# Kernel optimization log

Hardware: AMD Instinct MI355X
Metric: run time of the kernel (lower is better)

## Reference

```python
import jax, jax.numpy as jnp
import numpy as np

D = 1024      # d_model
H = 16        # num_heads
DK = D // H   # head dim = 64
C = 64        # chunk_size
MRP = 2 * C   # max_rel_pos = 128
B, S = 2, 2048


def setup_inputs() -> dict:
    key = jax.random.key(0)
    ks = jax.random.split(key, 7)
    s = 0.02
    x = jax.random.normal(ks[0], (B, S, D), jnp.float32)
    Wq = jax.random.normal(ks[1], (D, D), jnp.float32) * s
    Wk = jax.random.normal(ks[2], (D, D), jnp.float32) * s
    Wv = jax.random.normal(ks[3], (D, D), jnp.float32) * s
    Wo = jax.random.normal(ks[4], (D, D), jnp.float32) * s
    bq = jnp.zeros((D,), jnp.float32)
    bk = jnp.zeros((D,), jnp.float32)
    bv = jnp.zeros((D,), jnp.float32)
    bo = jnp.zeros((D,), jnp.float32)
    # torch init is zeros; use small values so the bias path is exercised
    rel_bias = jax.random.normal(ks[5], (2 * MRP + 1, H), jnp.float32) * s
    return dict(x=x, Wq=Wq, bq=bq, Wk=Wk, bk=bk, Wv=Wv, bv=bv, Wo=Wo, bo=bo,
                rel_bias=rel_bias)


def reference(x, Wq, bq, Wk, bk, Wv, bv, Wo, bo, rel_bias):
    b, s, _ = x.shape

    def heads(w, bias):
        return (x @ w + bias).reshape(b, s, H, DK).transpose(0, 2, 1, 3)  # [B,H,S,dk]

    Q = heads(Wq, bq)
    K = heads(Wk, bk)
    V = heads(Wv, bv)

    scale = jnp.sqrt(jnp.asarray(DK, x.dtype))
    scores = jnp.einsum('bhqd,bhkd->bhqk', Q, K) / scale  # [B,H,S,S]

    pos = jnp.arange(s)
    # chunked path's rel index reduces to global (q - k), clamped
    rel = jnp.clip(pos[:, None] - pos[None, :], -MRP, MRP) + MRP  # [S,S]
    bias2 = rel_bias[rel].transpose(2, 0, 1)  # [H,S,S]
    scores = scores + bias2[None]

    # growing-window chunk mask: query chunk i sees key chunks 0..i
    qc = pos // C
    allowed = qc[None, :] <= qc[:, None]  # [S_q, S_k]
    scores = jnp.where(allowed[None, None], scores, -jnp.inf)

    attn = jax.nn.softmax(scores, axis=-1)
    out = jnp.einsum('bhqk,bhkd->bhqd', attn, V)
    out = out.transpose(0, 2, 1, 3).reshape(b, s, D)
    return out @ Wo + bo
```

## Files before the change

### kernel.cpp

```cpp
#include <hip/hip_runtime.h>
#include <stdint.h>

#define NH 16
#define DKH 64
#define SEQ 2048
#define NBATCH 2
#define NROW (NBATCH*SEQ)
#define DM 1024
#define LOG2E 1.44269504088896f

typedef __attribute__((ext_vector_type(8))) __bf16 bf16x8;
typedef __attribute__((ext_vector_type(4))) __bf16 bf16x4;
typedef __attribute__((ext_vector_type(4))) float f32x4;

#if __has_builtin(__builtin_amdgcn_exp2f)
#define EXP2(x) __builtin_amdgcn_exp2f(x)
#else
#define EXP2(x) exp2f(x)
#endif

__device__ __forceinline__ unsigned short f2bf(float f) {
  union { float f; uint32_t u; } v; v.f = f;
  uint32_t r = v.u + 0x7FFFu + ((v.u >> 16) & 1u);
  return (unsigned short)(r >> 16);
}
__device__ __forceinline__ f32x4 mfma16(bf16x8 a, bf16x8 b, f32x4 c) {
  return __builtin_amdgcn_mfma_f32_16x16x32_bf16(a, b, c, 0, 0, 0);
}
__device__ __forceinline__ void gload_lds16(const void* g, void* l) {
  __builtin_amdgcn_global_load_lds(
      (__attribute__((address_space(1))) uint32_t*)(uintptr_t)g,
      (__attribute__((address_space(3))) uint32_t*)(uintptr_t)l,
      16, 0, 0);
}
__device__ __forceinline__ void barrier_raw() {
  asm volatile("" ::: "memory");
  __builtin_amdgcn_s_barrier();
  asm volatile("" ::: "memory");
}

__global__ __launch_bounds__(256) void k_cvt_x(const float* __restrict__ x,
                                               unsigned short* __restrict__ xb) {
  int i = blockIdx.x * 256 + threadIdx.x;
  float4 v = ((const float4*)x)[i];
  ushort4 o;
  o.x = f2bf(v.x); o.y = f2bf(v.y); o.z = f2bf(v.z); o.w = f2bf(v.w);
  ((ushort4*)xb)[i] = o;
}

__global__ __launch_bounds__(256) void k_cvt_w(
    const float* __restrict__ Wq, const float* __restrict__ Wk,
    const float* __restrict__ Wv, const float* __restrict__ Wo,
    unsigned short* __restrict__ Wqt, unsigned short* __restrict__ Wkt,
    unsigned short* __restrict__ Wvt, unsigned short* __restrict__ Wot) {
  __shared__ float tile[32][33];
  int z = blockIdx.z;
  const float* W = (z == 0) ? Wq : (z == 1) ? Wk : (z == 2) ? Wv : Wo;
  int ti = blockIdx.x, tj = blockIdx.y;
  int c = threadIdx.x & 31, r0 = threadIdx.x >> 5;
#pragma unroll
  for (int rr = 0; rr < 4; ++rr) {
    int r = r0 + rr * 8;
    tile[r][c] = W[(ti * 32 + r) * DM + tj * 32 + c];
  }
  __syncthreads();
  unsigned short* Out = (z == 0) ? Wqt : (z == 1) ? Wkt : (z == 2) ? Wvt : Wot;
#pragma unroll
  for (int rr = 0; rr < 4; ++rr) {
    int a = r0 + rr * 8;
    float v = tile[c][a];
    Out[(tj * 32 + a) * DM + ti * 32 + c] = f2bf(v);
  }
}

__global__ __launch_bounds__(256) void k_gemm_qkv(
    const unsigned short* __restrict__ xb,
    const unsigned short* __restrict__ Wqt, const unsigned short* __restrict__ Wkt,
    const unsigned short* __restrict__ Wvt,
    const float* __restrict__ bq, const float* __restrict__ bk,
    const float* __restrict__ bv,
    unsigned short* __restrict__ Q, unsigned short* __restrict__ Ko,
    unsigned short* __restrict__ Vt) {
  __shared__ __align__(16) unsigned short Al[2][128 * 64];
  __shared__ __align__(16) unsigned short Bl[2][128 * 64];
  int z = blockIdx.z;
  const unsigned short* Wt = (z == 0) ? Wqt : (z == 1) ? Wkt : Wvt;
  const float* bias = (z == 0) ? bq : (z == 1) ? bk : bv;

  int m0 = blockIdx.x * 128, n0 = blockIdx.y * 128;
  int tid = threadIdx.x, lane = tid & 63, wave = tid >> 6;
  int wr = wave >> 1, wc = wave & 1;
  int l15 = lane & 15, lg = lane >> 4;
  int r3 = lane >> 3, s3 = lane & 7;
  int gsw = (s3 ^ r3) << 4;
  int swz = l15 & 7;

  f32x4 acc[4][4] = {};

  auto stage = [&](int kb, int b) {
#pragma unroll
    for (int c = 0; c < 4; ++c) {
      int rb = c * 32 + wave * 8;
      gload_lds16((const char*)xb + (size_t)(m0 + rb + r3) * 2048 + kb * 128 + gsw,
                  (char*)&Al[b][0] + rb * 128);
      gload_lds16((const char*)Wt + (size_t)(n0 + rb + r3) * 2048 + kb * 128 + gsw,
                  (char*)&Bl[b][0] + rb * 128);
    }
  };

  stage(0, 0);
  stage(1, 1);

  for (int kb = 0; kb < 16; ++kb) {
    if (kb < 15) asm volatile("s_waitcnt vmcnt(8)" ::: "memory");
    else         asm volatile("s_waitcnt vmcnt(0)" ::: "memory");
    barrier_raw();
    int b = kb & 1;
#pragma unroll
    for (int ks = 0; ks < 2; ++ks) {
      int slot = lg + 4 * ks;
      int sofs = ((slot ^ swz) << 4);
      bf16x8 a[4], bfr[4];
#pragma unroll
      for (int mt = 0; mt < 4; ++mt)
        a[mt] = *(const bf16x8*)((const char*)&Al[b][0] + (wr * 64 + mt * 16 + l15) * 128 + sofs);
#pragma unroll
      for (int nt = 0; nt < 4; ++nt)
        bfr[nt] = *(const bf16x8*)((const char*)&Bl[b][0] + (wc * 64 + nt * 16 + l15) * 128 + sofs);
#pragma unroll
      for (int mt = 0; mt < 4; ++mt)
#pragma unroll
        for (int nt = 0; nt < 4; ++nt)
          acc[mt][nt] = mfma16(a[mt], bfr[nt], acc[mt][nt]);
    }
    barrier_raw();
    if (kb < 14) stage(kb + 2, b);
  }

#pragma unroll
  for (int nt = 0; nt < 4; ++nt) {
    int n = n0 + wc * 64 + nt * 16 + l15;
    float bb = bias[n];
    int h = n >> 6, dk = n & 63;
#pragma unroll
    for (int mt = 0; mt < 4; ++mt) {
      int mbase = m0 + wr * 64 + mt * 16 + lg * 4;
      int bidx = mbase >> 11, s = mbase & 2047;
      if (z < 2) {
        unsigned short* Out = (z == 0) ? Q : Ko;
#pragma unroll
        for (int r = 0; r < 4; ++r)
          Out[(((size_t)(bidx * NH + h)) * SEQ + s + r) * DKH + dk] =
              f2bf(acc[mt][nt][r] + bb);
      } else {
        ushort4 pk;
        pk.x = f2bf(acc[mt][nt][0] + bb);
        pk.y = f2bf(acc[mt][nt][1] + bb);
        pk.z = f2bf(acc[mt][nt][2] + bb);
        pk.w = f2bf(acc[mt][nt][3] + bb);
        *(ushort4*)&Vt[((size_t)(bidx * NH + h) * DKH + dk) * SEQ + s] = pk;
      }
    }
  }
}

__global__ __launch_bounds__(256) void k_attn(
    const unsigned short* __restrict__ Qg, const unsigned short* __restrict__ Kg,
    const unsigned short* __restrict__ Vtg, const float* __restrict__ rel_bias,
    unsigned short* __restrict__ AOh) {
  __shared__ __align__(16) unsigned short Kl[2][64 * 64];
  __shared__ __align__(16) unsigned short Vl[2][64 * 64];
  __shared__ float biasl[257];

  int blk = blockIdx.x;
  int bh = blk & 31;
  int qc = 31 - (blk >> 5);
  int h = bh & 15, bidx = bh >> 4;
  int tid = threadIdx.x, lane = tid & 63, wave = tid >> 6;
  int l15 = lane & 15, lg = lane >> 4;
  int r3 = lane >> 3, s3 = lane & 7;
  int gsw = (s3 ^ r3) * 16;

  const float C1L = 0.125f * LOG2E;

  for (int i = tid; i < 257; i += 256)
    biasl[i] = rel_bias[i * NH + h] * LOG2E - 6.0f * LOG2E;

  int qrow = qc * 64 + wave * 16 + l15;
  const unsigned short* qptr = Qg + ((size_t)bh * SEQ + qrow) * DKH + lg * 8;
  bf16x8 qf0 = *(const bf16x8*)(qptr);
  bf16x8 qf1 = *(const bf16x8*)(qptr + 32);

  const char* kcb = (const char*)(Kg + (size_t)bh * SEQ * DKH);
  const char* vcb = (const char*)(Vtg + (size_t)bh * DKH * SEQ);

  auto stage = [&](int j, int b) {
    const char* kj = kcb + (size_t)j * (64 * DKH * 2);
    const char* vj = vcb + (size_t)j * 128;
#pragma unroll
    for (int c = 0; c < 2; ++c) {
      int rb = wave * 16 + c * 8;
      gload_lds16(kj + (size_t)(rb + r3) * 128 + gsw,
                  (char*)&Kl[b][0] + rb * 128);
      gload_lds16(vj + (size_t)(rb + r3) * (SEQ * 2) + gsw,
                  (char*)&Vl[b][0] + rb * 128);
    }
  };

  float lsum = 0.f;
  f32x4 acc[4] = {};

  stage(0, 0);
  __syncthreads();
  float cfar = biasl[256];
  int swz = (l15 & 7);

  int vo[4];
#pragma unroll
  for (int kt = 0; kt < 4; ++kt)
    vo[kt] = (((kt * 2 + (lg >> 1)) ^ swz) << 4) + ((lg & 1) << 3);

  for (int j = 0; j <= qc; ++j) {
    int cur = j & 1;
    if (j < qc) stage(j + 1, cur ^ 1);

    const char* Kc = (const char*)&Kl[cur][0];
    const char* Vc = (const char*)&Vl[cur][0];

    f32x4 sa[4] = {};
    __builtin_amdgcn_s_setprio(1);
#pragma unroll
    for (int ks = 0; ks < 2; ++ks) {
      bf16x8 qa = ks ? qf1 : qf0;
      int slot = lg + 4 * ks;
#pragma unroll
      for (int kt = 0; kt < 4; ++kt) {
        bf16x8 kfr = *(const bf16x8*)(Kc + (kt * 16 + l15) * 128 + ((slot ^ swz) * 16));
        sa[kt] = mfma16(kfr, qa, sa[kt]);
      }
    }
    __builtin_amdgcn_s_setprio(0);

    float p[4][4];
    if (j >= qc - 2) {
      int kb0 = j * 64 + lg * 4;
#pragma unroll
      for (int kt = 0; kt < 4; ++kt)
#pragma unroll
        for (int r = 0; r < 4; ++r) {
          int rel = qrow - (kb0 + kt * 16 + r);
          rel = min(max(rel, -128), 128) + 128;
          p[kt][r] = EXP2(fmaf(sa[kt][r], C1L, biasl[rel]));
        }
    } else {
#pragma unroll
      for (int kt = 0; kt < 4; ++kt)
#pragma unroll
        for (int r = 0; r < 4; ++r)
          p[kt][r] = EXP2(fmaf(sa[kt][r], C1L, cfar));
    }
#pragma unroll
    for (int kt = 0; kt < 4; ++kt)
      lsum += (p[kt][0] + p[kt][1]) + (p[kt][2] + p[kt][3]);

    bf16x8 pfr0, pfr1;
#pragma unroll
    for (int jj = 0; jj < 4; ++jj) {
      pfr0[jj]     = (__bf16)p[0][jj];
      pfr0[jj + 4] = (__bf16)p[1][jj];
      pfr1[jj]     = (__bf16)p[2][jj];
      pfr1[jj + 4] = (__bf16)p[3][jj];
    }

    __builtin_amdgcn_s_setprio(1);
#pragma unroll
    for (int dt = 0; dt < 4; ++dt) {
      const char* vrow = Vc + (dt * 16 + l15) * 128;
      uint2 t0 = *(const uint2*)(vrow + vo[0]);
      uint2 t1 = *(const uint2*)(vrow + vo[1]);
      uint2 t2 = *(const uint2*)(vrow + vo[2]);
      uint2 t3 = *(const uint2*)(vrow + vo[3]);
      uint4 w0, w1;
      w0.x = t0.x; w0.y = t0.y; w0.z = t1.x; w0.w = t1.y;
      w1.x = t2.x; w1.y = t2.y; w1.z = t3.x; w1.w = t3.y;
      acc[dt] = mfma16(pfr0, *(const bf16x8*)&w0, acc[dt]);
      acc[dt] = mfma16(pfr1, *(const bf16x8*)&w1, acc[dt]);
    }
    __builtin_amdgcn_s_setprio(0);

    __syncthreads();
  }

  lsum += __shfl_xor(lsum, 16);
  lsum += __shfl_xor(lsum, 32);

#pragma unroll
  for (int r = 0; r < 4; ++r) {
    float inv = 1.0f / __shfl(lsum, lg * 4 + r, 64);
    int s = qc * 64 + wave * 16 + lg * 4 + r;
    size_t row = (size_t)bidx * SEQ + s;
#pragma unroll
    for (int dt = 0; dt < 4; ++dt) {
      float v = acc[dt][r] * inv;
      int col = h * 64 + dt * 16 + l15;
      AOh[row * DM + col] = f2bf(v);
    }
  }
}

__global__ __launch_bounds__(256) void k_gemm_out(
    const unsigned short* __restrict__ Ab, const unsigned short* __restrict__ Bt,
    const float* __restrict__ bo, float* __restrict__ out) {
  __shared__ __align__(16) unsigned short Al[2][128 * 64];
  __shared__ __align__(16) unsigned short Bl[2][128 * 64];

  int m0 = blockIdx.x * 128, n0 = blockIdx.y * 128;
  int tid = threadIdx.x, lane = tid & 63, wave = tid >> 6;
  int wr = wave >> 1, wc = wave & 1;
  int l15 = lane & 15, lg = lane >> 4;
  int r3 = lane >> 3, s3 = lane & 7;
  int gsw = (s3 ^ r3) << 4;
  int swz = l15 & 7;

  f32x4 acc[4][4] = {};

  auto stage = [&](int kb, int b) {
#pragma unroll
    for (int c = 0; c < 4; ++c) {
      int rb = c * 32 + wave * 8;
      gload_lds16((const char*)Ab + (size_t)(m0 + rb + r3) * 2048 + kb * 128 + gsw,
                  (char*)&Al[b][0] + rb * 128);
      gload_lds16((const char*)Bt + (size_t)(n0 + rb + r3) * 2048 + kb * 128 + gsw,
                  (char*)&Bl[b][0] + rb * 128);
    }
  };

  stage(0, 0);
  stage(1, 1);

  for (int kb = 0; kb < 16; ++kb) {
    if (kb < 15) asm volatile("s_waitcnt vmcnt(8)" ::: "memory");
    else         asm volatile("s_waitcnt vmcnt(0)" ::: "memory");
    barrier_raw();
    int b = kb & 1;
#pragma unroll
    for (int ks = 0; ks < 2; ++ks) {
      int slot = lg + 4 * ks;
      int sofs = ((slot ^ swz) << 4);
      bf16x8 a[4], bfr[4];
#pragma unroll
      for (int mt = 0; mt < 4; ++mt)
        a[mt] = *(const bf16x8*)((const char*)&Al[b][0] + (wr * 64 + mt * 16 + l15) * 128 + sofs);
#pragma unroll
      for (int nt = 0; nt < 4; ++nt)
        bfr[nt] = *(const bf16x8*)((const char*)&Bl[b][0] + (wc * 64 + nt * 16 + l15) * 128 + sofs);
#pragma unroll
      for (int mt = 0; mt < 4; ++mt)
#pragma unroll
        for (int nt = 0; nt < 4; ++nt)
          acc[mt][nt] = mfma16(a[mt], bfr[nt], acc[mt][nt]);
    }
    barrier_raw();
    if (kb < 14) stage(kb + 2, b);
  }

#pragma unroll
  for (int nt = 0; nt < 4; ++nt) {
    int n = n0 + wc * 64 + nt * 16 + l15;
    float bb = bo[n];
#pragma unroll
    for (int mt = 0; mt < 4; ++mt) {
      int mbase = m0 + wr * 64 + mt * 16 + lg * 4;
#pragma unroll
      for (int r = 0; r < 4; ++r)
        out[(size_t)(mbase + r) * DM + n] = acc[mt][nt][r] + bb;
    }
  }
}

extern "C" void kernel_launch(void* const* d_in, const int* in_sizes, int n_in,
                              void* d_out, int out_size, void* d_ws, size_t ws_size,
                              hipStream_t stream) {
  const float* x  = (const float*)d_in[0];
  const float* Wq = (const float*)d_in[1];
  const float* bq = (const float*)d_in[2];
  const float* Wk = (const float*)d_in[3];
  const float* bk = (const float*)d_in[4];
  const float* Wv = (const float*)d_in[5];
  const float* bv = (const float*)d_in[6];
  const float* Wo = (const float*)d_in[7];
  const float* bo = (const float*)d_in[8];
  const float* rb = (const float*)d_in[9];
  float* out = (float*)d_out;

  char* ws = (char*)d_ws;
  size_t off = 0;
  auto alloc = [&](size_t bytes) {
    char* p = ws + off; off += (bytes + 255) & ~(size_t)255; return p;
  };
  unsigned short* xb   = (unsigned short*)alloc((size_t)NROW * DM * 2);
  unsigned short* Wqt  = (unsigned short*)alloc((size_t)DM * DM * 2);
  unsigned short* Wkt  = (unsigned short*)alloc((size_t)DM * DM * 2);
  unsigned short* Wvt  = (unsigned short*)alloc((size_t)DM * DM * 2);
  unsigned short* Wot  = (unsigned short*)alloc((size_t)DM * DM * 2);
  unsigned short* Qb   = (unsigned short*)alloc((size_t)NROW * DM * 2);
  unsigned short* Kb   = (unsigned short*)alloc((size_t)NROW * DM * 2);
  unsigned short* Vtb  = (unsigned short*)alloc((size_t)NROW * DM * 2);
  unsigned short* AOh  = (unsigned short*)alloc((size_t)NROW * DM * 2);

  k_cvt_x<<<dim3(NROW * DM / 4 / 256), dim3(256), 0, stream>>>(x, xb);
  k_cvt_w<<<dim3(32, 32, 4), dim3(256), 0, stream>>>(Wq, Wk, Wv, Wo,
                                                     Wqt, Wkt, Wvt, Wot);
  k_gemm_qkv<<<dim3(32, 8, 3), dim3(256), 0, stream>>>(xb, Wqt, Wkt, Wvt,
                                                       bq, bk, bv, Qb, Kb, Vtb);
  k_attn<<<dim3(1024), dim3(256), 0, stream>>>(Qb, Kb, Vtb, rb, AOh);
  k_gemm_out<<<dim3(32, 8), dim3(256), 0, stream>>>(AOh, Wot, bo, out);
}
```

Before: 104.4 us.

## Split long attention query chunks across two blocks and merge with normalize kernel

```diff
diff --git a/kernel.cpp b/kernel.cpp
--- a/kernel.cpp
+++ b/kernel.cpp
@@ -24,6 +24,10 @@
   uint32_t r = v.u + 0x7FFFu + ((v.u >> 16) & 1u);
   return (unsigned short)(r >> 16);
 }
+__device__ __forceinline__ float bf2f(unsigned short b) {
+  union { uint32_t u; float f; } v; v.u = ((uint32_t)b) << 16;
+  return v.f;
+}
 __device__ __forceinline__ f32x4 mfma16(bf16x8 a, bf16x8 b, f32x4 c) {
   return __builtin_amdgcn_mfma_f32_16x16x32_bf16(a, b, c, 0, 0, 0);
 }
@@ -51,8 +55,7 @@
 __global__ __launch_bounds__(256) void k_cvt_w(
     const float* __restrict__ Wq, const float* __restrict__ Wk,
     const float* __restrict__ Wv, const float* __restrict__ Wo,
-    unsigned short* __restrict__ Wqt, unsigned short* __restrict__ Wkt,
-    unsigned short* __restrict__ Wvt, unsigned short* __restrict__ Wot) {
+    unsigned short* __restrict__ Wcat, unsigned short* __restrict__ Wot) {
   __shared__ float tile[32][33];
   int z = blockIdx.z;
   const float* W = (z == 0) ? Wq : (z == 1) ? Wk : (z == 2) ? Wv : Wo;
@@ -64,7 +67,7 @@
     tile[r][c] = W[(ti * 32 + r) * DM + tj * 32 + c];
   }
   __syncthreads();
-  unsigned short* Out = (z == 0) ? Wqt : (z == 1) ? Wkt : (z == 2) ? Wvt : Wot;
+  unsigned short* Out = (z < 3) ? (Wcat + (size_t)z * DM * DM) : Wot;
 #pragma unroll
   for (int rr = 0; rr < 4; ++rr) {
     int a = r0 + rr * 8;
@@ -73,19 +76,21 @@
   }
 }
 
+__global__ __launch_bounds__(256) void k_bias(
+    const float* __restrict__ bq, const float* __restrict__ bk,
+    const float* __restrict__ bv, float* __restrict__ bc) {
+  int i = blockIdx.x * 256 + threadIdx.x;
+  bc[i] = (i < 1024) ? bq[i] : (i < 2048) ? bk[i - 1024] : bv[i - 2048];
+}
+
 __global__ __launch_bounds__(256) void k_gemm_qkv(
     const unsigned short* __restrict__ xb,
-    const unsigned short* __restrict__ Wqt, const unsigned short* __restrict__ Wkt,
-    const unsigned short* __restrict__ Wvt,
-    const float* __restrict__ bq, const float* __restrict__ bk,
-    const float* __restrict__ bv,
+    const unsigned short* __restrict__ Wcat,
+    const float* __restrict__ bias,
     unsigned short* __restrict__ Q, unsigned short* __restrict__ Ko,
     unsigned short* __restrict__ Vt) {
   __shared__ __align__(16) unsigned short Al[2][128 * 64];
   __shared__ __align__(16) unsigned short Bl[2][128 * 64];
-  int z = blockIdx.z;
-  const unsigned short* Wt = (z == 0) ? Wqt : (z == 1) ? Wkt : Wvt;
-  const float* bias = (z == 0) ? bq : (z == 1) ? bk : bv;
 
   int m0 = blockIdx.x * 128, n0 = blockIdx.y * 128;
   int tid = threadIdx.x, lane = tid & 63, wave = tid >> 6;
@@ -103,7 +108,7 @@
       int rb = c * 32 + wave * 8;
       gload_lds16((const char*)xb + (size_t)(m0 + rb + r3) * 2048 + kb * 128 + gsw,
                   (char*)&Al[b][0] + rb * 128);
-      gload_lds16((const char*)Wt + (size_t)(n0 + rb + r3) * 2048 + kb * 128 + gsw,
+      gload_lds16((const char*)Wcat + (size_t)(n0 + rb + r3) * 2048 + kb * 128 + gsw,
                   (char*)&Bl[b][0] + rb * 128);
     }
   };
@@ -141,7 +146,8 @@
   for (int nt = 0; nt < 4; ++nt) {
     int n = n0 + wc * 64 + nt * 16 + l15;
     float bb = bias[n];
-    int h = n >> 6, dk = n & 63;
+    int z = n >> 10, nn = n & 1023;
+    int h = nn >> 6, dk = nn & 63;
 #pragma unroll
     for (int mt = 0; mt < 4; ++mt) {
       int mbase = m0 + wr * 64 + mt * 16 + lg * 4;
@@ -167,14 +173,26 @@
 __global__ __launch_bounds__(256) void k_attn(
     const unsigned short* __restrict__ Qg, const unsigned short* __restrict__ Kg,
     const unsigned short* __restrict__ Vtg, const float* __restrict__ rel_bias,
-    unsigned short* __restrict__ AOh) {
+    unsigned short* __restrict__ Pp0, unsigned short* __restrict__ Pp1,
+    float* __restrict__ L0, float* __restrict__ L1) {
   __shared__ __align__(16) unsigned short Kl[2][64 * 64];
   __shared__ __align__(16) unsigned short Vl[2][64 * 64];
   __shared__ float biasl[257];
 
   int blk = blockIdx.x;
   int bh = blk & 31;
-  int qc = 31 - (blk >> 5);
+  int p = blk >> 5;
+  int qc, j0;
+  if (p < 16)       { qc = 16 + p; j0 = 0;  }
+  else if (p == 16) { qc = 31;     j0 = 16; }
+  else if (p == 17) { qc = 15;     j0 = 0;  }
+  else {
+    int k = (p - 18) >> 1;
+    if (((p - 18) & 1) == 0) { qc = 30 - k; j0 = 16; }
+    else                     { qc = 14 - k; j0 = 0;  }
+  }
+  int cnt = (j0 == 0) ? (qc < 16 ? qc + 1 : 16) : (qc - 15);
+
   int h = bh & 15, bidx = bh >> 4;
   int tid = threadIdx.x, lane = tid & 63, wave = tid >> 6;
   int l15 = lane & 15, lg = lane >> 4;
@@ -210,7 +228,7 @@
   float lsum = 0.f;
   f32x4 acc[4] = {};
 
-  stage(0, 0);
+  stage(j0, 0);
   __syncthreads();
   float cfar = biasl[256];
   int swz = (l15 & 7);
@@ -220,9 +238,10 @@
   for (int kt = 0; kt < 4; ++kt)
     vo[kt] = (((kt * 2 + (lg >> 1)) ^ swz) << 4) + ((lg & 1) << 3);
 
-  for (int j = 0; j <= qc; ++j) {
-    int cur = j & 1;
-    if (j < qc) stage(j + 1, cur ^ 1);
+  for (int jj = 0; jj < cnt; ++jj) {
+    int j = j0 + jj;
+    int cur = jj & 1;
+    if (jj + 1 < cnt) stage(j + 1, cur ^ 1);
 
     const char* Kc = (const char*)&Kl[cur][0];
     const char* Vc = (const char*)&Vl[cur][0];
@@ -241,7 +260,7 @@
     }
     __builtin_amdgcn_s_setprio(0);
 
-    float p[4][4];
+    float pp[4][4];
     if (j >= qc - 2) {
       int kb0 = j * 64 + lg * 4;
 #pragma unroll
@@ -250,26 +269,26 @@
         for (int r = 0; r < 4; ++r) {
           int rel = qrow - (kb0 + kt * 16 + r);
           rel = min(max(rel, -128), 128) + 128;
-          p[kt][r] = EXP2(fmaf(sa[kt][r], C1L, biasl[rel]));
+          pp[kt][r] = EXP2(fmaf(sa[kt][r], C1L, biasl[rel]));
         }
     } else {
 #pragma unroll
       for (int kt = 0; kt < 4; ++kt)
 #pragma unroll
         for (int r = 0; r < 4; ++r)
-          p[kt][r] = EXP2(fmaf(sa[kt][r], C1L, cfar));
+          pp[kt][r] = EXP2(fmaf(sa[kt][r], C1L, cfar));
     }
 #pragma unroll
     for (int kt = 0; kt < 4; ++kt)
-      lsum += (p[kt][0] + p[kt][1]) + (p[kt][2] + p[kt][3]);
+      lsum += (pp[kt][0] + pp[kt][1]) + (pp[kt][2] + pp[kt][3]);
 
     bf16x8 pfr0, pfr1;
 #pragma unroll
-    for (int jj = 0; jj < 4; ++jj) {
-      pfr0[jj]     = (__bf16)p[0][jj];
-      pfr0[jj + 4] = (__bf16)p[1][jj];
-      pfr1[jj]     = (__bf16)p[2][jj];
-      pfr1[jj + 4] = (__bf16)p[3][jj];
+    for (int jjj = 0; jjj < 4; ++jjj) {
+      pfr0[jjj]     = (__bf16)pp[0][jjj];
+      pfr0[jjj + 4] = (__bf16)pp[1][jjj];
+      pfr1[jjj]     = (__bf16)pp[2][jjj];
+      pfr1[jjj + 4] = (__bf16)pp[3][jjj];
     }
 
     __builtin_amdgcn_s_setprio(1);
@@ -294,18 +313,48 @@
   lsum += __shfl_xor(lsum, 16);
   lsum += __shfl_xor(lsum, 32);
 
+  unsigned short* Pb = (j0 == 0) ? Pp0 : Pp1;
+  float* Lb = (j0 == 0) ? L0 : L1;
+
+  if (lg == 0)
+    Lb[(size_t)bh * SEQ + qc * 64 + wave * 16 + l15] = lsum;
+
 #pragma unroll
   for (int r = 0; r < 4; ++r) {
-    float inv = 1.0f / __shfl(lsum, lg * 4 + r, 64);
     int s = qc * 64 + wave * 16 + lg * 4 + r;
     size_t row = (size_t)bidx * SEQ + s;
 #pragma unroll
     for (int dt = 0; dt < 4; ++dt) {
-      float v = acc[dt][r] * inv;
       int col = h * 64 + dt * 16 + l15;
-      AOh[row * DM + col] = f2bf(v);
-    }
-  }
+      Pb[row * DM + col] = f2bf(acc[dt][r]);
+    }
+  }
+}
+
+__global__ __launch_bounds__(256) void k_norm(
+    const unsigned short* __restrict__ Pp0, const unsigned short* __restrict__ Pp1,
+    const float* __restrict__ L0, const float* __restrict__ L1,
+    unsigned short* __restrict__ AOh) {
+  int row = blockIdx.x;
+  int t = threadIdx.x;
+  int s = row & (SEQ - 1), bidx = row >> 11;
+  int qc = s >> 6;
+  int col = t * 4;
+  int h = col >> 6;
+  size_t li = (size_t)(bidx * NH + h) * SEQ + s;
+  ushort4 a = *(const ushort4*)&Pp0[(size_t)row * DM + col];
+  float v0 = bf2f(a.x), v1 = bf2f(a.y), v2 = bf2f(a.z), v3 = bf2f(a.w);
+  float l = L0[li];
+  if (qc >= 16) {
+    ushort4 b = *(const ushort4*)&Pp1[(size_t)row * DM + col];
+    v0 += bf2f(b.x); v1 += bf2f(b.y); v2 += bf2f(b.z); v3 += bf2f(b.w);
+    l += L1[li];
+  }
+  float inv = 1.0f / l;
+  ushort4 o;
+  o.x = f2bf(v0 * inv); o.y = f2bf(v1 * inv);
+  o.z = f2bf(v2 * inv); o.w = f2bf(v3 * inv);
+  *(ushort4*)&AOh[(size_t)row * DM + col] = o;
 }
 
 __global__ __launch_bounds__(256) void k_gemm_out(
@@ -399,20 +448,23 @@
     char* p = ws + off; off += (bytes + 255) & ~(size_t)255; return p;
   };
   unsigned short* xb   = (unsigned short*)alloc((size_t)NROW * DM * 2);
-  unsigned short* Wqt  = (unsigned short*)alloc((size_t)DM * DM * 2);
-  unsigned short* Wkt  = (unsigned short*)alloc((size_t)DM * DM * 2);
-  unsigned short* Wvt  = (unsigned short*)alloc((size_t)DM * DM * 2);
+  unsigned short* Wcat = (unsigned short*)alloc((size_t)3 * DM * DM * 2);
   unsigned short* Wot  = (unsigned short*)alloc((size_t)DM * DM * 2);
+  float*          bc   = (float*)alloc((size_t)3 * DM * 4);
   unsigned short* Qb   = (unsigned short*)alloc((size_t)NROW * DM * 2);
   unsigned short* Kb   = (unsigned short*)alloc((size_t)NROW * DM * 2);
   unsigned short* Vtb  = (unsigned short*)alloc((size_t)NROW * DM * 2);
-  unsigned short* AOh  = (unsigned short*)alloc((size_t)NROW * DM * 2);
+  unsigned short* Pp0  = (unsigned short*)alloc((size_t)NROW * DM * 2);
+  unsigned short* Pp1  = (unsigned short*)alloc((size_t)NROW * DM * 2);
+  float*          L0   = (float*)alloc((size_t)32 * SEQ * 4);
+  float*          L1   = (float*)alloc((size_t)32 * SEQ * 4);
+  unsigned short* AOh  = xb;
 
   k_cvt_x<<<dim3(NROW * DM / 4 / 256), dim3(256), 0, stream>>>(x, xb);
-  k_cvt_w<<<dim3(32, 32, 4), dim3(256), 0, stream>>>(Wq, Wk, Wv, Wo,
-                                                     Wqt, Wkt, Wvt, Wot);
-  k_gemm_qkv<<<dim3(32, 8, 3), dim3(256), 0, stream>>>(xb, Wqt, Wkt, Wvt,
-                                                       bq, bk, bv, Qb, Kb, Vtb);
-  k_attn<<<dim3(1024), dim3(256), 0, stream>>>(Qb, Kb, Vtb, rb, AOh);
+  k_cvt_w<<<dim3(32, 32, 4), dim3(256), 0, stream>>>(Wq, Wk, Wv, Wo, Wcat, Wot);
+  k_bias<<<dim3(12), dim3(256), 0, stream>>>(bq, bk, bv, bc);
+  k_gemm_qkv<<<dim3(32, 24), dim3(256), 0, stream>>>(xb, Wcat, bc, Qb, Kb, Vtb);
+  k_attn<<<dim3(1536), dim3(256), 0, stream>>>(Qb, Kb, Vtb, rb, Pp0, Pp1, L0, L1);
+  k_norm<<<dim3(4096), dim3(256), 0, stream>>>(Pp0, Pp1, L0, L1, AOh);
   k_gemm_out<<<dim3(32, 8), dim3(256), 0, stream>>>(AOh, Wot, bo, out);
 }
```

New measurement: 110.0 us. 5.3% more time.
